# Kernel optimization log

Hardware: AMD Instinct MI355X
Metric: run time of the kernel (lower is better)

Reference implementation:

```python
import jax, jax.numpy as jnp
import numpy as np

N_HEADS = 16
HEAD_DIM = 128
EPS = 1e-6


def _rmsnorm(t, w):
    # RMSNorm over last dim (head_dim)
    var = jnp.mean(jnp.square(t), axis=-1, keepdims=True)
    return t * jax.lax.rsqrt(var + EPS) * w


def _apply_rope(t, freqs):
    # t: [b, s, h, d]; freqs: [s, 1, d//2, 2, 2]
    b, s, h, d = t.shape
    t2 = t.reshape(b, s, h, 2, d // 2)
    t_ = jnp.moveaxis(t2, -2, -1)[..., None, :].astype(jnp.float32)  # [b,s,h,d/2,1,2]
    out = freqs[..., 0] * t_[..., 0] + freqs[..., 1] * t_[..., 1]    # [b,s,h,d/2,2]
    out = jnp.moveaxis(out, -1, -2).reshape(b, s, h, d)
    return out.astype(t.dtype)


def setup_inputs() -> dict:
    key = jax.random.key(0)
    ks = jax.random.split(key, 8)
    B, S, D = 2, 2048, 2048
    inner = N_HEADS * HEAD_DIM
    sc = 1.0 / np.sqrt(D)
    return {
        "x": jax.random.normal(ks[0], (B, S, D), jnp.float32),
        "rope_emb": jax.random.normal(ks[1], (S, 1, HEAD_DIM // 2, 2, 2), jnp.float32),
        "Wq": jax.random.normal(ks[2], (inner, D), jnp.float32) * sc,
        "Wk": jax.random.normal(ks[3], (inner, D), jnp.float32) * sc,
        "Wv": jax.random.normal(ks[4], (inner, D), jnp.float32) * sc,
        "Wo": jax.random.normal(ks[5], (D, inner), jnp.float32) * sc,
        "q_norm_w": jnp.ones((HEAD_DIM,), jnp.float32),
        "k_norm_w": jnp.ones((HEAD_DIM,), jnp.float32),
    }


def reference(x, rope_emb, Wq, Wk, Wv, Wo, q_norm_w, k_norm_w):
    b, s, _ = x.shape
    h, d = N_HEADS, HEAD_DIM
    q = (x @ Wq.T).reshape(b, s, h, d)
    k = (x @ Wk.T).reshape(b, s, h, d)
    v = (x @ Wv.T).reshape(b, s, h, d)
    q = _apply_rope(_rmsnorm(q, q_norm_w), rope_emb)
    k = _apply_rope(_rmsnorm(k, k_norm_w), rope_emb)
    # SDPA, heads-first layout
    qh = jnp.transpose(q, (0, 2, 1, 3))  # [b,h,s,d]
    kh = jnp.transpose(k, (0, 2, 1, 3))
    vh = jnp.transpose(v, (0, 2, 1, 3))
    scale = 1.0 / np.sqrt(d)
    scores = jnp.einsum('bhqd,bhkd->bhqk', qh, kh) * scale
    attn = jax.nn.softmax(scores, axis=-1)
    out = jnp.einsum('bhqk,bhkd->bhqd', attn, vh)  # [b,h,s,d]
    out = jnp.transpose(out, (0, 2, 1, 3)).reshape(b, s, h * d)
    return out @ Wo.T
```

## Files before the change

### kernel.cpp

```cpp
#include <hip/hip_runtime.h>
#include <hip/hip_bf16.h>
#include <stdint.h>

typedef __bf16 bf16;
typedef __bf16 bf16x4 __attribute__((ext_vector_type(4)));
typedef __bf16 bf16x8 __attribute__((ext_vector_type(8)));
typedef float f32x4 __attribute__((ext_vector_type(4)));
typedef float f32x16 __attribute__((ext_vector_type(16)));

#define N_HEADS 16
#define HEAD_DIM 128
#define SEQ 2048
#define DIM 2048
#define BATCH 2
#define MROWS (BATCH * SEQ)
#define NQKV (3 * DIM)
#define SM_SCALE 0.08838834764831845f
#define SMAX 24.0f

__device__ __forceinline__ bf16 f2b(float f) {
  union { __hip_bfloat16 h; bf16 b; } u;
  u.h = __float2bfloat16(f);
  return u.b;
}

__device__ __forceinline__ uint32_t pack2(float a, float b) {
  union { __hip_bfloat16 h; unsigned short s; } ua, ub;
  ua.h = __float2bfloat16(a); ub.h = __float2bfloat16(b);
  return (uint32_t)ua.s | ((uint32_t)ub.s << 16);
}

__device__ __forceinline__ void async16(const bf16* g, bf16* l) {
  __builtin_amdgcn_global_load_lds(
      (__attribute__((address_space(1))) void*)(uintptr_t)g,
      (__attribute__((address_space(3))) void*)(uintptr_t)l,
      16, 0, 0);
}

__global__ __launch_bounds__(256) void cvt_kernel(const float* __restrict__ src,
                                                  bf16* __restrict__ dst, int n) {
  int i = (blockIdx.x * 256 + threadIdx.x) * 8;
  if (i >= n) return;
  float4 a = *(const float4*)(src + i);
  float4 b = *(const float4*)(src + i + 4);
  bf16x8 o;
  o[0] = f2b(a.x); o[1] = f2b(a.y); o[2] = f2b(a.z); o[3] = f2b(a.w);
  o[4] = f2b(b.x); o[5] = f2b(b.y); o[6] = f2b(b.z); o[7] = f2b(b.w);
  *(bf16x8*)(dst + i) = o;
}

__global__ __launch_bounds__(256) void cvt_w4(const float* __restrict__ w0,
                                              const float* __restrict__ w1,
                                              const float* __restrict__ w2,
                                              const float* __restrict__ w3,
                                              bf16* __restrict__ wqkv,
                                              bf16* __restrict__ wo) {
  const int per = (DIM * DIM) / 8 / 256;
  int which = blockIdx.x / per;
  int i = (blockIdx.x % per) * 256 * 8 + threadIdx.x * 8;
  const float* src = which == 0 ? w0 : which == 1 ? w1 : which == 2 ? w2 : w3;
  bf16* dst = which < 3 ? wqkv + (size_t)which * DIM * DIM : wo;
  float4 a = *(const float4*)(src + i);
  float4 b = *(const float4*)(src + i + 4);
  bf16x8 o;
  o[0] = f2b(a.x); o[1] = f2b(a.y); o[2] = f2b(a.z); o[3] = f2b(a.w);
  o[4] = f2b(b.x); o[5] = f2b(b.y); o[6] = f2b(b.z); o[7] = f2b(b.w);
  *(bf16x8*)(dst + i) = o;
}

__device__ __forceinline__ void gemm_tile_mainloop(
    const bf16* __restrict__ A, const bf16* __restrict__ Bw, int K,
    int rowBase, int colBase, bf16* lA, bf16* lB, f32x4 acc[4][4]) {
  const int t = threadIdx.x;
  const int w = t >> 6, lane = t & 63;
  const int lm = lane & 15, quad = lane >> 4;
  const int wr = (w >> 1) * 64, wc = (w & 1) * 64;

  for (int kt = 0; kt < K; kt += 32) {
#pragma unroll
    for (int i = 0; i < 2; i++) {
      const int c = i * 256 + t;
      const int r = c >> 2, cc = (c & 3) << 3;
      async16(A + (size_t)(rowBase + r) * K + (kt + cc), lA + (i * 256 + w * 64) * 8);
      async16(Bw + (size_t)(colBase + r) * K + (kt + cc), lB + (i * 256 + w * 64) * 8);
    }
    asm volatile("s_waitcnt vmcnt(0)" ::: "memory");
    __syncthreads();
    bf16x8 af[4], bfr[4];
#pragma unroll
    for (int f = 0; f < 4; f++)
      af[f] = *(const bf16x8*)(lA + (wr + f * 16 + lm) * 32 + quad * 8);
#pragma unroll
    for (int f = 0; f < 4; f++)
      bfr[f] = *(const bf16x8*)(lB + (wc + f * 16 + lm) * 32 + quad * 8);
#pragma unroll
    for (int fr = 0; fr < 4; fr++)
#pragma unroll
      for (int fc = 0; fc < 4; fc++)
        acc[fr][fc] = __builtin_amdgcn_mfma_f32_16x16x32_bf16(af[fr], bfr[fc], acc[fr][fc], 0, 0, 0);
    __syncthreads();
  }
}

__global__ __launch_bounds__(256) void gemm_qkv(const bf16* __restrict__ X,
                                                const bf16* __restrict__ W,
                                                bf16* __restrict__ Q,
                                                bf16* __restrict__ Kv,
                                                bf16* __restrict__ VT) {
  __shared__ __align__(16) bf16 lA[128 * 32];
  __shared__ __align__(16) bf16 lB[128 * 32];
  f32x4 acc[4][4];
  f32x4 z = {0.f, 0.f, 0.f, 0.f};
#pragma unroll
  for (int i = 0; i < 4; i++)
#pragma unroll
    for (int j = 0; j < 4; j++) acc[i][j] = z;

  const int rowBase = blockIdx.y * 128, colBase = blockIdx.x * 128;
  gemm_tile_mainloop(X, W, DIM, rowBase, colBase, lA, lB, acc);

  const int t = threadIdx.x, w = t >> 6, lane = t & 63;
  const int lm = lane & 15, quad = lane >> 4;
  const int wr = (w >> 1) * 64, wc = (w & 1) * 64;
  const int which = colBase >> 11;
  if (which < 2) {
    bf16* dst = which ? Kv : Q;
#pragma unroll
    for (int fr = 0; fr < 4; fr++)
#pragma unroll
      for (int fc = 0; fc < 4; fc++)
#pragma unroll
        for (int r = 0; r < 4; r++) {
          int m = rowBase + wr + fr * 16 + quad * 4 + r;
          int n = (colBase + wc + fc * 16 + lm) & 2047;
          int h = n >> 7, d = n & 127;
          int b = m >> 11, s = m & 2047;
          dst[(((size_t)(b * N_HEADS + h) * SEQ) + s) * HEAD_DIM + d] = f2b(acc[fr][fc][r]);
        }
  } else {
#pragma unroll
    for (int fr = 0; fr < 4; fr++)
#pragma unroll
      for (int fc = 0; fc < 4; fc++) {
        int n = (colBase + wc + fc * 16 + lm) & 2047;
        int h = n >> 7, d = n & 127;
        int m = rowBase + wr + fr * 16 + quad * 4;
        int b = m >> 11, s = m & 2047;
        bf16x4 pk;
#pragma unroll
        for (int r = 0; r < 4; r++) pk[r] = f2b(acc[fr][fc][r]);
        *(bf16x4*)&VT[((size_t)(b * N_HEADS + h) * HEAD_DIM + d) * SEQ + s] = pk;
      }
  }
}

__global__ __launch_bounds__(256) void gemm_out(const bf16* __restrict__ A,
                                                const bf16* __restrict__ W,
                                                float* __restrict__ out) {
  __shared__ __align__(16) bf16 lA[128 * 32];
  __shared__ __align__(16) bf16 lB[128 * 32];
  f32x4 acc[4][4];
  f32x4 z = {0.f, 0.f, 0.f, 0.f};
#pragma unroll
  for (int i = 0; i < 4; i++)
#pragma unroll
    for (int j = 0; j < 4; j++) acc[i][j] = z;

  const int rowBase = blockIdx.y * 128, colBase = blockIdx.x * 128;
  gemm_tile_mainloop(A, W, DIM, rowBase, colBase, lA, lB, acc);

  const int t = threadIdx.x, w = t >> 6, lane = t & 63;
  const int lm = lane & 15, quad = lane >> 4;
  const int wr = (w >> 1) * 64, wc = (w & 1) * 64;
#pragma unroll
  for (int fr = 0; fr < 4; fr++)
#pragma unroll
    for (int fc = 0; fc < 4; fc++)
#pragma unroll
      for (int r = 0; r < 4; r++) {
        int m = rowBase + wr + fr * 16 + quad * 4 + r;
        int n = colBase + wc + fc * 16 + lm;
        out[(size_t)m * DIM + n] = acc[fr][fc][r];
      }
}

__global__ __launch_bounds__(256) void norm_rope(bf16* __restrict__ Q,
                                                 bf16* __restrict__ K,
                                                 const float* __restrict__ rope,
                                                 const float* __restrict__ qw,
                                                 const float* __restrict__ kw) {
  const int t = threadIdx.x, w = t >> 6, lane = t & 63;
  const int rid = blockIdx.x * 4 + w;
  const int which = rid >> 16;
  const int row = rid & 65535;
  bf16* ptr = (which ? K : Q) + (size_t)row * HEAD_DIM;
  const float* nw = which ? kw : qw;
  const int s = row & (SEQ - 1);

  float x0 = (float)ptr[lane];
  float x1 = (float)ptr[lane + 64];
  float ss = x0 * x0 + x1 * x1;
#pragma unroll
  for (int off = 32; off; off >>= 1) ss += __shfl_xor(ss, off);
  float r = rsqrtf(ss * (1.f / 128.f) + 1e-6f);
  float x0n = x0 * r * nw[lane];
  float x1n = x1 * r * nw[lane + 64];
  float4 f = ((const float4*)rope)[s * 64 + lane];
  float y0 = f.x * x0n + f.y * x1n;
  float y1 = f.z * x0n + f.w * x1n;
  if (!which) { y0 *= SM_SCALE; y1 *= SM_SCALE; }
  ptr[lane] = f2b(y0);
  ptr[lane + 64] = f2b(y1);
}

__global__ __launch_bounds__(256, 2) void attn_kernel(const bf16* __restrict__ Q,
                                                      const bf16* __restrict__ K,
                                                      const bf16* __restrict__ VT,
                                                      bf16* __restrict__ O) {
  __shared__ __align__(16) bf16 Ks[64 * 128];
  __shared__ __align__(16) bf16 Vs[128 * 64];

  const int t = threadIdx.x, w = t >> 6, lane = t & 63;
  const int lq = lane & 31, h = lane >> 5;
  const int qh = w >> 1, kb = w & 1;
  const int bh = blockIdx.x, qt = blockIdx.y;

  bf16x8 qf[2][8];
#pragma unroll
  for (int qs = 0; qs < 2; qs++) {
    const bf16* Qp = Q + ((size_t)bh * SEQ + qt * 128 + qh * 64 + qs * 32 + lq) * HEAD_DIM;
#pragma unroll
    for (int ks = 0; ks < 8; ks++)
      qf[qs][ks] = *(const bf16x8*)(Qp + ks * 16 + h * 8);
  }

  f32x16 oacc[2][4];
#pragma unroll
  for (int qs = 0; qs < 2; qs++)
#pragma unroll
    for (int nb = 0; nb < 4; nb++)
#pragma unroll
      for (int e = 0; e < 16; e++) oacc[qs][nb][e] = 0.f;
  float rsum[2] = {0.f, 0.f};

  const bf16* kbase = K + (size_t)bh * SEQ * HEAD_DIM;
  const bf16* vbase = VT + (size_t)bh * HEAD_DIM * SEQ;
  const int kr = kb * 32 + lq;

  const int krow = w * 16 + (lane >> 4), kcc = lane & 15;
  const int vrow = w * 32 + (lane >> 3), vcc = lane & 7;
  bf16x8 kreg[4], vreg[4];

  auto load_tile = [&](int j) {
    const bf16* kp = kbase + (size_t)j * 64 * HEAD_DIM;
    const bf16* vp = vbase + j * 64;
#pragma unroll
    for (int i = 0; i < 4; i++)
      kreg[i] = *(const bf16x8*)(kp + (krow + i * 4) * HEAD_DIM + kcc * 8);
#pragma unroll
    for (int i = 0; i < 4; i++)
      vreg[i] = *(const bf16x8*)(vp + (size_t)(vrow + i * 8) * SEQ + vcc * 8);
  };

  load_tile(0);

  for (int j = 0; j < SEQ / 64; j++) {
#pragma unroll
    for (int i = 0; i < 4; i++) {
      int r = krow + i * 4;
      *(bf16x8*)&Ks[r * 128 + ((kcc ^ (r & 15)) << 3)] = kreg[i];
    }
#pragma unroll
    for (int i = 0; i < 4; i++) {
      int d = vrow + i * 8;
      *(bf16x8*)&Vs[d * 64 + ((vcc ^ (d & 7)) << 3)] = vreg[i];
    }
    __syncthreads();

    if (j + 1 < SEQ / 64) load_tile(j + 1);

    f32x16 sacc[2];
#pragma unroll
    for (int qs = 0; qs < 2; qs++)
#pragma unroll
      for (int e = 0; e < 16; e++) sacc[qs][e] = -SMAX;
#pragma unroll
    for (int ks = 0; ks < 8; ks++) {
      int c = ks * 2 + h;
      bf16x8 kf = *(const bf16x8*)&Ks[kr * 128 + ((c ^ (kr & 15)) << 3)];
      sacc[0] = __builtin_amdgcn_mfma_f32_32x32x16_bf16(kf, qf[0][ks], sacc[0], 0, 0, 0);
      sacc[1] = __builtin_amdgcn_mfma_f32_32x32x16_bf16(kf, qf[1][ks], sacc[1], 0, 0, 0);
    }

    uint32_t a1[2][4], a2[2][4];
#pragma unroll
    for (int qs = 0; qs < 2; qs++) {
      float e[16];
#pragma unroll
      for (int r = 0; r < 16; r++) {
        e[r] = __expf(sacc[qs][r]);
        rsum[qs] += e[r];
      }
      uint32_t pk[8];
#pragma unroll
      for (int i = 0; i < 8; i++) pk[i] = pack2(e[2 * i], e[2 * i + 1]);
      uint32_t ta = h ? pk[0] : pk[2], tb = h ? pk[1] : pk[3];
      uint32_t tc = h ? pk[4] : pk[6], td = h ? pk[5] : pk[7];
      uint32_t ra = __shfl_xor((int)ta, 32), rb = __shfl_xor((int)tb, 32);
      uint32_t rc = __shfl_xor((int)tc, 32), rd = __shfl_xor((int)td, 32);
      a1[qs][0] = h ? ra : pk[0]; a1[qs][1] = h ? rb : pk[1];
      a1[qs][2] = h ? pk[2] : ra; a1[qs][3] = h ? pk[3] : rb;
      a2[qs][0] = h ? rc : pk[4]; a2[qs][1] = h ? rd : pk[5];
      a2[qs][2] = h ? pk[6] : rc; a2[qs][3] = h ? pk[7] : rd;
    }

#pragma unroll
    for (int ks2 = 0; ks2 < 2; ks2++) {
      union { uint32_t u[4]; bf16x8 v; } ap0, ap1;
#pragma unroll
      for (int i = 0; i < 4; i++) {
        ap0.u[i] = ks2 ? a2[0][i] : a1[0][i];
        ap1.u[i] = ks2 ? a2[1][i] : a1[1][i];
      }
      int c2 = kb * 4 + ks2 * 2 + h;
#pragma unroll
      for (int nb = 0; nb < 4; nb++) {
        int rv = nb * 32 + lq;
        bf16x8 bv = *(const bf16x8*)&Vs[rv * 64 + ((c2 ^ (rv & 7)) << 3)];
        oacc[0][nb] = __builtin_amdgcn_mfma_f32_32x32x16_bf16(ap0.v, bv, oacc[0][nb], 0, 0, 0);
        oacc[1][nb] = __builtin_amdgcn_mfma_f32_32x32x16_bf16(ap1.v, bv, oacc[1][nb], 0, 0, 0);
      }
    }
    __syncthreads();
  }

  rsum[0] += __shfl_xor(rsum[0], 32);
  rsum[1] += __shfl_xor(rsum[1], 32);
  float* Om = (float*)&Ks[0];
  float* Rs = (float*)&Vs[0];
  const int pair = qh;
  const int b = bh >> 4, hh = bh & 15;
  float inv[2] = {0.f, 0.f};

#pragma unroll
  for (int nb = 0; nb < 4; nb++) {
    if (kb == 1) {
      if (nb == 0 && h == 0) {
        Rs[(pair * 2 + 0) * 32 + lq] = rsum[0];
        Rs[(pair * 2 + 1) * 32 + lq] = rsum[1];
      }
#pragma unroll
      for (int qs = 0; qs < 2; qs++)
#pragma unroll
        for (int r = 0; r < 16; r++) {
          int rowm = (r & 3) + 8 * (r >> 2) + 4 * h;
          Om[(pair * 64 + qs * 32 + rowm) * 32 + lq] = oacc[qs][nb][r];
        }
    }
    __syncthreads();
    if (kb == 0) {
      if (nb == 0) {
        inv[0] = 1.f / (rsum[0] + Rs[(pair * 2 + 0) * 32 + lq]);
        inv[1] = 1.f / (rsum[1] + Rs[(pair * 2 + 1) * 32 + lq]);
      }
#pragma unroll
      for (int qs = 0; qs < 2; qs++)
#pragma unroll
        for (int r = 0; r < 16; r++) {
          int rowm = (r & 3) + 8 * (r >> 2) + 4 * h;
          float val = oacc[qs][nb][r] + Om[(pair * 64 + qs * 32 + rowm) * 32 + lq];
          float iv = __shfl(inv[qs], rowm);
          int qg = qt * 128 + qh * 64 + qs * 32 + rowm;
          O[((size_t)b * SEQ + qg) * DIM + hh * HEAD_DIM + nb * 32 + lq] = f2b(val * iv);
        }
    }
    __syncthreads();
  }
}

extern "C" void kernel_launch(void* const* d_in, const int* in_sizes, int n_in,
                              void* d_out, int out_size, void* d_ws, size_t ws_size,
                              hipStream_t stream) {
  const float* x    = (const float*)d_in[0];
  const float* rope = (const float*)d_in[1];
  const float* Wq   = (const float*)d_in[2];
  const float* Wk   = (const float*)d_in[3];
  const float* Wv   = (const float*)d_in[4];
  const float* Wo   = (const float*)d_in[5];
  const float* qw   = (const float*)d_in[6];
  const float* kw   = (const float*)d_in[7];
  float* out = (float*)d_out;

  char* ws = (char*)d_ws;
  bf16* xb   = (bf16*)ws;
  bf16* wqkv = (bf16*)(ws + (16u << 20));
  bf16* wo   = (bf16*)(ws + (40u << 20));
  bf16* qb   = (bf16*)(ws + (48u << 20));
  bf16* kb   = (bf16*)(ws + (64u << 20));
  bf16* vt   = (bf16*)(ws + (80u << 20));
  bf16* attn = xb;

  const int NX = MROWS * DIM;
  const int NW = DIM * DIM;

  cvt_kernel<<<NX / 8 / 256, 256, 0, stream>>>(x, xb, NX);
  cvt_w4<<<4 * (NW / 8 / 256), 256, 0, stream>>>(Wq, Wk, Wv, Wo, wqkv, wo);

  gemm_qkv<<<dim3(NQKV / 128, MROWS / 128), 256, 0, stream>>>(xb, wqkv, qb, kb, vt);
  norm_rope<<<(2 * BATCH * N_HEADS * SEQ) / 4, 256, 0, stream>>>(qb, kb, rope, qw, kw);
  attn_kernel<<<dim3(BATCH * N_HEADS, SEQ / 128), 256, 0, stream>>>(qb, kb, vt, attn);
  gemm_out<<<dim3(DIM / 128, MROWS / 128), 256, 0, stream>>>(attn, wo, out);
}
```

Baseline: 452.1 us.

## Load K/V MFMA fragments directly from global memory, dropping LDS staging

The attention kernel no longer stages K and V tiles through shared memory with swizzling and per-tile barriers. Each wave now loads its own MFMA operand fragments for K and transposed V straight from global memory every iteration. This removes LDS traffic and the two __syncthreads per tile. In exchange, waves sharing a block reload the same K/V data, so global/L2 traffic grows, and the software prefetch of the next tile is gone, which can expose load latency.

```diff
diff --git a/kernel.cpp b/kernel.cpp
--- a/kernel.cpp
+++ b/kernel.cpp
@@ -217,8 +217,8 @@
                                                       const bf16* __restrict__ K,
                                                       const bf16* __restrict__ VT,
                                                       bf16* __restrict__ O) {
-  __shared__ __align__(16) bf16 Ks[64 * 128];
-  __shared__ __align__(16) bf16 Vs[128 * 64];
+  __shared__ __align__(16) float Om[2 * 64 * 32];
+  __shared__ float Rs[2 * 2 * 32];
 
   const int t = threadIdx.x, w = t >> 6, lane = t & 63;
   const int lq = lane & 31, h = lane >> 5;
@@ -243,41 +243,15 @@
       for (int e = 0; e < 16; e++) oacc[qs][nb][e] = 0.f;
   float rsum[2] = {0.f, 0.f};
 
-  const bf16* kbase = K + (size_t)bh * SEQ * HEAD_DIM;
-  const bf16* vbase = VT + (size_t)bh * HEAD_DIM * SEQ;
   const int kr = kb * 32 + lq;
-
-  const int krow = w * 16 + (lane >> 4), kcc = lane & 15;
-  const int vrow = w * 32 + (lane >> 3), vcc = lane & 7;
-  bf16x8 kreg[4], vreg[4];
-
-  auto load_tile = [&](int j) {
-    const bf16* kp = kbase + (size_t)j * 64 * HEAD_DIM;
-    const bf16* vp = vbase + j * 64;
-#pragma unroll
-    for (int i = 0; i < 4; i++)
-      kreg[i] = *(const bf16x8*)(kp + (krow + i * 4) * HEAD_DIM + kcc * 8);
-#pragma unroll
-    for (int i = 0; i < 4; i++)
-      vreg[i] = *(const bf16x8*)(vp + (size_t)(vrow + i * 8) * SEQ + vcc * 8);
-  };
-
-  load_tile(0);
+  const bf16* kfp = K + (size_t)bh * SEQ * HEAD_DIM + (size_t)kr * HEAD_DIM + h * 8;
+  const bf16* vfp = VT + (size_t)bh * HEAD_DIM * SEQ + (size_t)lq * SEQ + kb * 32 + h * 8;
 
   for (int j = 0; j < SEQ / 64; j++) {
-#pragma unroll
-    for (int i = 0; i < 4; i++) {
-      int r = krow + i * 4;
-      *(bf16x8*)&Ks[r * 128 + ((kcc ^ (r & 15)) << 3)] = kreg[i];
-    }
-#pragma unroll
-    for (int i = 0; i < 4; i++) {
-      int d = vrow + i * 8;
-      *(bf16x8*)&Vs[d * 64 + ((vcc ^ (d & 7)) << 3)] = vreg[i];
-    }
-    __syncthreads();
-
-    if (j + 1 < SEQ / 64) load_tile(j + 1);
+    bf16x8 kf[8];
+#pragma unroll
+    for (int ks = 0; ks < 8; ks++)
+      kf[ks] = *(const bf16x8*)(kfp + (size_t)j * 64 * HEAD_DIM + ks * 16);
 
     f32x16 sacc[2];
 #pragma unroll
@@ -286,11 +260,16 @@
       for (int e = 0; e < 16; e++) sacc[qs][e] = -SMAX;
 #pragma unroll
     for (int ks = 0; ks < 8; ks++) {
-      int c = ks * 2 + h;
-      bf16x8 kf = *(const bf16x8*)&Ks[kr * 128 + ((c ^ (kr & 15)) << 3)];
-      sacc[0] = __builtin_amdgcn_mfma_f32_32x32x16_bf16(kf, qf[0][ks], sacc[0], 0, 0, 0);
-      sacc[1] = __builtin_amdgcn_mfma_f32_32x32x16_bf16(kf, qf[1][ks], sacc[1], 0, 0, 0);
-    }
+      sacc[0] = __builtin_amdgcn_mfma_f32_32x32x16_bf16(kf[ks], qf[0][ks], sacc[0], 0, 0, 0);
+      sacc[1] = __builtin_amdgcn_mfma_f32_32x32x16_bf16(kf[ks], qf[1][ks], sacc[1], 0, 0, 0);
+    }
+
+    bf16x8 bv[4][2];
+#pragma unroll
+    for (int nb = 0; nb < 4; nb++)
+#pragma unroll
+      for (int ks2 = 0; ks2 < 2; ks2++)
+        bv[nb][ks2] = *(const bf16x8*)(vfp + (size_t)nb * 32 * SEQ + j * 64 + ks2 * 16);
 
     uint32_t a1[2][4], a2[2][4];
 #pragma unroll
@@ -322,22 +301,16 @@
         ap0.u[i] = ks2 ? a2[0][i] : a1[0][i];
         ap1.u[i] = ks2 ? a2[1][i] : a1[1][i];
       }
-      int c2 = kb * 4 + ks2 * 2 + h;
 #pragma unroll
       for (int nb = 0; nb < 4; nb++) {
-        int rv = nb * 32 + lq;
-        bf16x8 bv = *(const bf16x8*)&Vs[rv * 64 + ((c2 ^ (rv & 7)) << 3)];
-        oacc[0][nb] = __builtin_amdgcn_mfma_f32_32x32x16_bf16(ap0.v, bv, oacc[0][nb], 0, 0, 0);
-        oacc[1][nb] = __builtin_amdgcn_mfma_f32_32x32x16_bf16(ap1.v, bv, oacc[1][nb], 0, 0, 0);
-      }
-    }
-    __syncthreads();
+        oacc[0][nb] = __builtin_amdgcn_mfma_f32_32x32x16_bf16(ap0.v, bv[nb][ks2], oacc[0][nb], 0, 0, 0);
+        oacc[1][nb] = __builtin_amdgcn_mfma_f32_32x32x16_bf16(ap1.v, bv[nb][ks2], oacc[1][nb], 0, 0, 0);
+      }
+    }
   }
 
   rsum[0] += __shfl_xor(rsum[0], 32);
   rsum[1] += __shfl_xor(rsum[1], 32);
-  float* Om = (float*)&Ks[0];
-  float* Rs = (float*)&Vs[0];
   const int pair = qh;
   const int b = bh >> 4, hh = bh & 15;
   float inv[2] = {0.f, 0.f};
```

After: 523.0 us. 1.16x slower.
